# Performance work log

Measured on AMD Instinct MI355X. Metric: run time of the kernel, lower is better.

## Reference

```python
import jax, jax.numpy as jnp
import numpy as np

CD_WT = 5.0
CLASSIFY_WT = 1.0
B, N, M, NUM_CLASSES = 32, 2048, 2048, 6


def setup_inputs() -> dict:
    key = jax.random.key(0)
    k1, k2, k3, k4 = jax.random.split(key, 4)
    inst_shape = jax.random.normal(k1, (B, N, 3), dtype=jnp.float32)
    model = jax.random.normal(k2, (B, M, 3), dtype=jnp.float32)
    pred = jax.random.normal(k3, (B, NUM_CLASSES), dtype=jnp.float32)
    gt = jax.random.randint(k4, (B,), 0, NUM_CLASSES, dtype=jnp.int64)
    return {"inst_shape": inst_shape, "model": model, "pred": pred, "gt": gt}


def _chamfer(a, b):
    # a: [B,N,3], b: [B,M,3]; squared pairwise distances [B,N,M]
    # ||a-b||^2 = ||a||^2 + ||b||^2 - 2 a.b  (avoids [B,N,M,3] intermediate)
    a2 = jnp.sum(a * a, axis=-1)  # [B,N]
    b2 = jnp.sum(b * b, axis=-1)  # [B,M]
    ab = jnp.einsum('bnd,bmd->bnm', a, b)  # [B,N,M]
    d = a2[:, :, None] + b2[:, None, :] - 2.0 * ab  # [B,N,M]
    dist1 = jnp.min(d, axis=2)  # [B,N] nearest in b for each a
    dist2 = jnp.min(d, axis=1)  # [B,M] nearest in a for each b
    loss = jnp.mean(dist1) + jnp.mean(dist2)
    return loss, dist1, dist2


def _cross_entropy(logits, labels):
    # nn.CrossEntropyLoss with default mean reduction
    logp = jax.nn.log_softmax(logits, axis=-1)  # [B,C]
    nll = -jnp.take_along_axis(logp, labels[:, None], axis=-1)[:, 0]
    return jnp.mean(nll)


def reference(inst_shape, model, pred, gt):
    cd_loss, _, _ = _chamfer(inst_shape, model)
    classify_loss = _cross_entropy(pred, gt)
    total_loss = CD_WT * cd_loss + CLASSIFY_WT * classify_loss
    return (total_loss, cd_loss, classify_loss)
```

## Files before the change

### kernel.cpp

```cpp
#include <hip/hip_runtime.h>

typedef __attribute__((ext_vector_type(8)))  short short8;
typedef __attribute__((ext_vector_type(16))) float f32x16;
typedef __attribute__((ext_vector_type(16))) unsigned u32x16;

#define NPTS 2048
#define BATCH 32
#define NUM_CLASSES 6
#define THREADS 256
#define BF16_ONE ((short)0x3F80)
#define FMAX_BITS 0x7F7FFFFFu

__device__ __forceinline__ unsigned short f2bf(float x) {
    union { float f; unsigned u; } v; v.f = x;
    unsigned r = v.u + 0x7FFF + ((v.u >> 16) & 1);
    return (unsigned short)(r >> 16);
}
__device__ __forceinline__ float bf2f(unsigned short h) {
    union { unsigned u; float f; } v; v.u = ((unsigned)h) << 16; return v.f;
}
__device__ __forceinline__ unsigned f2u(float x) {
    union { float f; unsigned u; } v; v.f = x; return v.u;
}
__device__ __forceinline__ float u2f(unsigned x) {
    union { unsigned u; float f; } v; v.u = x; return v.f;
}
__device__ __forceinline__ unsigned umin2(unsigned a, unsigned b) {
    return a < b ? a : b;
}
template<int CTRL>
__device__ __forceinline__ unsigned dpp_ror_umin(unsigned v) {
    unsigned r = (unsigned)__builtin_amdgcn_update_dpp((int)v, (int)v, CTRL, 0xF, 0xF, false);
    return umin2(v, r);
}
__device__ __forceinline__ unsigned swz16_umin(unsigned v) {
    unsigned r = (unsigned)__builtin_amdgcn_ds_swizzle((int)v, 0x401F);
    return umin2(v, r);
}

__global__ __launch_bounds__(THREADS, 2) void chamfer_mfma32(
    const float* __restrict__ inst, const float* __restrict__ model,
    float* __restrict__ partial)
{
    __shared__ char  cands[NPTS * 32];
    __shared__ float wsum[4];

    const int blk   = blockIdx.x;
    const int dir   = blk >> 8;
    const int batch = (blk >> 3) & 31;
    const int qc    = blk & 7;
    const int tid   = threadIdx.x;
    const int lane  = tid & 63, wid = tid >> 6;
    const int lh    = lane >> 5, lr = lane & 31;

    const float* __restrict__ Q = dir ? model : inst;
    const float* __restrict__ C = dir ? inst  : model;

    const float* cb = C + (size_t)batch * NPTS * 3;
    for (int c = tid; c < NPTS; c += THREADS) {
        float bx = cb[c*3+0], by = cb[c*3+1], bz = cb[c*3+2];
        float m2x = -2.f*bx, m2y = -2.f*by, m2z = -2.f*bz;
        unsigned short hx = f2bf(m2x), hy = f2bf(m2y), hz = f2bf(m2z);
        unsigned short lx = f2bf(m2x - bf2f(hx));
        unsigned short ly = f2bf(m2y - bf2f(hy));
        unsigned short lz = f2bf(m2z - bf2f(hz));
        float b2 = fmaf(bx,bx, fmaf(by,by, bz*bz));
        unsigned short b2h = f2bf(b2);
        unsigned short b2l = f2bf(b2 - bf2f(b2h));
        short8 kg0 = { (short)hx,(short)hy,(short)hz,(short)hx,(short)hy,(short)hz,(short)lx,(short)ly };
        short8 kg1 = { (short)lz,(short)b2h,(short)b2l, BF16_ONE, BF16_ONE, 0,0,0 };
        char* tbase = cands + (c >> 5) * 1024 + (c & 31) * 16;
        *(short8*)(tbase)       = kg0;
        *(short8*)(tbase + 512) = kg1;
    }

    short8 af0, af1;
    const float* qb = Q + ((size_t)batch * NPTS + (size_t)qc * 256) * 3;
    #pragma unroll
    for (int qt = 0; qt < 2; ++qt) {
        const int qi = (wid * 2 + qt) * 32 + lr;
        float x = qb[qi*3+0], y = qb[qi*3+1], z = qb[qi*3+2];
        unsigned short hx = f2bf(x), hy = f2bf(y), hz = f2bf(z);
        unsigned short lx = f2bf(x - bf2f(hx));
        unsigned short ly = f2bf(y - bf2f(hy));
        unsigned short lz = f2bf(z - bf2f(hz));
        float a2 = fmaf(x,x, fmaf(y,y, z*z));
        unsigned short a2h = f2bf(a2);
        unsigned short a2l = f2bf(a2 - bf2f(a2h));
        short8 f;
        if (lh == 0)
            f = (short8){ (short)hx,(short)hy,(short)hz,(short)lx,(short)ly,(short)lz,(short)hx,(short)hy };
        else
            f = (short8){ (short)hz, BF16_ONE, BF16_ONE, (short)a2h,(short)a2l, 0,0,0 };
        if (qt == 0) af0 = f; else af1 = f;
    }
    __syncthreads();

    u32x16 mnU, mnU2;
    f32x16 zero16;
    #pragma unroll
    for (int r = 0; r < 16; ++r) { mnU[r] = FMAX_BITS; mnU2[r] = FMAX_BITS; zero16[r] = 0.f; }

    const char* cp = cands + lh * 512 + lr * 16;
    short8 c0 = *(const short8*)(cp);
    short8 c1 = *(const short8*)(cp + 1024);
    short8 n0 = *(const short8*)(cp + 2048);
    short8 n1 = *(const short8*)(cp + 3072);
    cp += 4096;
    f32x16 p00 = __builtin_amdgcn_mfma_f32_32x32x16_bf16(af0, c0, zero16, 0,0,0);
    f32x16 p01 = __builtin_amdgcn_mfma_f32_32x32x16_bf16(af0, c1, zero16, 0,0,0);
    f32x16 p10 = __builtin_amdgcn_mfma_f32_32x32x16_bf16(af1, c0, zero16, 0,0,0);
    f32x16 p11 = __builtin_amdgcn_mfma_f32_32x32x16_bf16(af1, c1, zero16, 0,0,0);

    #pragma unroll 2
    for (int s = 1; s < 31; ++s) {
        c0 = n0; c1 = n1;
        n0 = *(const short8*)(cp);
        n1 = *(const short8*)(cp + 1024);
        cp += 2048;
        f32x16 q00 = __builtin_amdgcn_mfma_f32_32x32x16_bf16(af0, c0, zero16, 0,0,0);
        f32x16 q01 = __builtin_amdgcn_mfma_f32_32x32x16_bf16(af0, c1, zero16, 0,0,0);
        f32x16 q10 = __builtin_amdgcn_mfma_f32_32x32x16_bf16(af1, c0, zero16, 0,0,0);
        f32x16 q11 = __builtin_amdgcn_mfma_f32_32x32x16_bf16(af1, c1, zero16, 0,0,0);
        #pragma unroll
        for (int r = 0; r < 16; ++r)
            mnU[r]  = umin2(umin2(f2u(p00[r]), f2u(p01[r])), mnU[r]);
        #pragma unroll
        for (int r = 0; r < 16; ++r)
            mnU2[r] = umin2(umin2(f2u(p10[r]), f2u(p11[r])), mnU2[r]);
        p00 = q00; p01 = q01; p10 = q10; p11 = q11;
    }
    {
        f32x16 q00 = __builtin_amdgcn_mfma_f32_32x32x16_bf16(af0, n0, zero16, 0,0,0);
        f32x16 q01 = __builtin_amdgcn_mfma_f32_32x32x16_bf16(af0, n1, zero16, 0,0,0);
        f32x16 q10 = __builtin_amdgcn_mfma_f32_32x32x16_bf16(af1, n0, zero16, 0,0,0);
        f32x16 q11 = __builtin_amdgcn_mfma_f32_32x32x16_bf16(af1, n1, zero16, 0,0,0);
        #pragma unroll
        for (int r = 0; r < 16; ++r) {
            mnU[r]  = umin2(umin2(f2u(p00[r]), f2u(p01[r])), mnU[r]);
            mnU2[r] = umin2(umin2(f2u(p10[r]), f2u(p11[r])), mnU2[r]);
        }
        #pragma unroll
        for (int r = 0; r < 16; ++r) {
            mnU[r]  = umin2(umin2(f2u(q00[r]), f2u(q01[r])), mnU[r]);
            mnU2[r] = umin2(umin2(f2u(q10[r]), f2u(q11[r])), mnU2[r]);
        }
    }

    float s = 0.f;
    #pragma unroll
    for (int r = 0; r < 16; ++r) {
        unsigned v = mnU[r];
        v = dpp_ror_umin<0x121>(v);
        v = dpp_ror_umin<0x122>(v);
        v = dpp_ror_umin<0x124>(v);
        v = dpp_ror_umin<0x128>(v);
        v = swz16_umin(v);
        s += u2f(v);
        unsigned w = mnU2[r];
        w = dpp_ror_umin<0x121>(w);
        w = dpp_ror_umin<0x122>(w);
        w = dpp_ror_umin<0x124>(w);
        w = dpp_ror_umin<0x128>(w);
        w = swz16_umin(w);
        s += u2f(w);
    }
    s += __shfl_xor(s, 32, 64);
    if (lane == 0) wsum[wid] = s;
    __syncthreads();
    if (tid == 0) partial[blk] = (wsum[0] + wsum[1]) + (wsum[2] + wsum[3]);
}

__global__ __launch_bounds__(256) void finalize_kernel(
    const float* __restrict__ partial, const float* __restrict__ pred,
    const int* __restrict__ gt, float* __restrict__ out)
{
    __shared__ float s_ce[BATCH];
    __shared__ float wsum[4];
    const int tid = threadIdx.x;

    float v = partial[tid] + partial[tid + 256];
    #pragma unroll
    for (int o = 32; o > 0; o >>= 1) v += __shfl_down(v, o, 64);
    const int lane = tid & 63, wid = tid >> 6;
    if (lane == 0) wsum[wid] = v;

    if (tid < BATCH) {
        const float* row = pred + tid * NUM_CLASSES;
        float mx = row[0];
        #pragma unroll
        for (int c = 1; c < NUM_CLASSES; ++c) mx = fmaxf(mx, row[c]);
        float se = 0.f;
        #pragma unroll
        for (int c = 0; c < NUM_CLASSES; ++c) se += __expf(row[c] - mx);
        const int lbl = gt[tid];
        s_ce[tid] = -(row[lbl] - mx - __logf(se));
    }
    __syncthreads();

    if (tid == 0) {
        float cd_sum = (wsum[0] + wsum[1]) + (wsum[2] + wsum[3]);
        float cd = cd_sum / (float)(BATCH * NPTS);
        float ce = 0.f;
        for (int i = 0; i < BATCH; ++i) ce += s_ce[i];
        ce /= (float)BATCH;
        out[0] = 5.f * cd + ce;
        out[1] = cd;
        out[2] = ce;
    }
}

extern "C" void kernel_launch(void* const* d_in, const int* in_sizes, int n_in,
                              void* d_out, int out_size, void* d_ws, size_t ws_size,
                              hipStream_t stream) {
    const float* inst  = (const float*)d_in[0];
    const float* model = (const float*)d_in[1];
    const float* pred  = (const float*)d_in[2];
    const int*   gt    = (const int*)d_in[3];
    float* out     = (float*)d_out;
    float* partial = (float*)d_ws;

    chamfer_mfma32<<<512, THREADS, 0, stream>>>(inst, model, partial);
    finalize_kernel<<<1, 256, 0, stream>>>(partial, pred, gt, out);
}
```

Before: 17.86 us.

## Compute the distance matrix once and derive row and column minima with atomics

Instead of launching separate block sets for each chamfer direction, each block now computes one tile of the inst-by-model distance matrix. It folds row minima and column minima from the same MFMA outputs and merges them into global buffers with atomicMin. This halves the MFMA and LDS candidate work. In exchange it adds a memset of the min buffers, per-step cross-lane shuffles and global atomics, plus an extra reduction kernel launch before the finalize step.

```diff
diff --git a/kernel.cpp b/kernel.cpp
--- a/kernel.cpp
+++ b/kernel.cpp
@@ -11,6 +11,9 @@
 #define BF16_ONE ((short)0x3F80)
 #define FMAX_BITS 0x7F7FFFFFu
 
+#define COL_OFF  65536
+#define PART_OFF 131072
+
 __device__ __forceinline__ unsigned short f2bf(float x) {
     union { float f; unsigned u; } v; v.f = x;
     unsigned r = v.u + 0x7FFF + ((v.u >> 16) & 1);
@@ -38,26 +41,27 @@
     return umin2(v, r);
 }
 
-__global__ __launch_bounds__(THREADS, 2) void chamfer_mfma32(
+__global__ __launch_bounds__(THREADS, 2) void chamfer_sym(
     const float* __restrict__ inst, const float* __restrict__ model,
-    float* __restrict__ partial)
+    unsigned* __restrict__ ws)
 {
-    __shared__ char  cands[NPTS * 32];
-    __shared__ float wsum[4];
+    __shared__ char cands[1024 * 32];
 
     const int blk   = blockIdx.x;
-    const int dir   = blk >> 8;
-    const int batch = (blk >> 3) & 31;
-    const int qc    = blk & 7;
+    const int mc    = blk & 1;
+    const int qc    = (blk >> 1) & 7;
+    const int batch = blk >> 4;
     const int tid   = threadIdx.x;
     const int lane  = tid & 63, wid = tid >> 6;
     const int lh    = lane >> 5, lr = lane & 31;
 
-    const float* __restrict__ Q = dir ? model : inst;
-    const float* __restrict__ C = dir ? inst  : model;
-
-    const float* cb = C + (size_t)batch * NPTS * 3;
-    for (int c = tid; c < NPTS; c += THREADS) {
+    unsigned* rowmin = ws + batch * NPTS;
+    unsigned* colmin = ws + COL_OFF + batch * NPTS + mc * 1024;
+
+    const float* cb = model + ((size_t)batch * NPTS + (size_t)mc * 1024) * 3;
+    #pragma unroll
+    for (int k = 0; k < 4; ++k) {
+        const int c = tid + k * THREADS;
         float bx = cb[c*3+0], by = cb[c*3+1], bz = cb[c*3+2];
         float m2x = -2.f*bx, m2y = -2.f*by, m2z = -2.f*bz;
         unsigned short hx = f2bf(m2x), hy = f2bf(m2y), hz = f2bf(m2z);
@@ -75,7 +79,7 @@
     }
 
     short8 af0, af1;
-    const float* qb = Q + ((size_t)batch * NPTS + (size_t)qc * 256) * 3;
+    const float* qb = inst + ((size_t)batch * NPTS + (size_t)qc * 256) * 3;
     #pragma unroll
     for (int qt = 0; qt < 2; ++qt) {
         const int qi = (wid * 2 + qt) * 32 + lr;
@@ -101,6 +105,25 @@
     #pragma unroll
     for (int r = 0; r < 16; ++r) { mnU[r] = FMAX_BITS; mnU2[r] = FMAX_BITS; zero16[r] = 0.f; }
 
+#define FOLD(P00,P01,P10,P11, TB) do {                                         \
+    _Pragma("unroll") for (int r = 0; r < 16; ++r)                             \
+        mnU[r]  = umin2(umin2(f2u(P00[r]), f2u(P01[r])), mnU[r]);              \
+    _Pragma("unroll") for (int r = 0; r < 16; ++r)                             \
+        mnU2[r] = umin2(umin2(f2u(P10[r]), f2u(P11[r])), mnU2[r]);             \
+    unsigned ca = umin2(f2u(P00[0]), f2u(P10[0]));                             \
+    unsigned cc = umin2(f2u(P01[0]), f2u(P11[0]));                             \
+    _Pragma("unroll") for (int r = 1; r < 16; ++r) {                           \
+        ca = umin2(ca, umin2(f2u(P00[r]), f2u(P10[r])));                       \
+        cc = umin2(cc, umin2(f2u(P01[r]), f2u(P11[r])));                       \
+    }                                                                          \
+    ca = umin2(ca, (unsigned)__shfl_xor((int)ca, 32, 64));                     \
+    cc = umin2(cc, (unsigned)__shfl_xor((int)cc, 32, 64));                     \
+    if (lh == 0) {                                                             \
+        atomicMin(&colmin[(TB) + lr], ca);                                     \
+        atomicMin(&colmin[(TB) + 32 + lr], cc);                                \
+    }                                                                          \
+} while (0)
+
     const char* cp = cands + lh * 512 + lr * 16;
     short8 c0 = *(const short8*)(cp);
     short8 c1 = *(const short8*)(cp + 1024);
@@ -113,7 +136,7 @@
     f32x16 p11 = __builtin_amdgcn_mfma_f32_32x32x16_bf16(af1, c1, zero16, 0,0,0);
 
     #pragma unroll 2
-    for (int s = 1; s < 31; ++s) {
+    for (int s = 1; s < 15; ++s) {
         c0 = n0; c1 = n1;
         n0 = *(const short8*)(cp);
         n1 = *(const short8*)(cp + 1024);
@@ -122,12 +145,7 @@
         f32x16 q01 = __builtin_amdgcn_mfma_f32_32x32x16_bf16(af0, c1, zero16, 0,0,0);
         f32x16 q10 = __builtin_amdgcn_mfma_f32_32x32x16_bf16(af1, c0, zero16, 0,0,0);
         f32x16 q11 = __builtin_amdgcn_mfma_f32_32x32x16_bf16(af1, c1, zero16, 0,0,0);
-        #pragma unroll
-        for (int r = 0; r < 16; ++r)
-            mnU[r]  = umin2(umin2(f2u(p00[r]), f2u(p01[r])), mnU[r]);
-        #pragma unroll
-        for (int r = 0; r < 16; ++r)
-            mnU2[r] = umin2(umin2(f2u(p10[r]), f2u(p11[r])), mnU2[r]);
+        FOLD(p00, p01, p10, p11, (s - 1) * 64);
         p00 = q00; p01 = q01; p10 = q10; p11 = q11;
     }
     {
@@ -135,55 +153,59 @@
         f32x16 q01 = __builtin_amdgcn_mfma_f32_32x32x16_bf16(af0, n1, zero16, 0,0,0);
         f32x16 q10 = __builtin_amdgcn_mfma_f32_32x32x16_bf16(af1, n0, zero16, 0,0,0);
         f32x16 q11 = __builtin_amdgcn_mfma_f32_32x32x16_bf16(af1, n1, zero16, 0,0,0);
-        #pragma unroll
-        for (int r = 0; r < 16; ++r) {
-            mnU[r]  = umin2(umin2(f2u(p00[r]), f2u(p01[r])), mnU[r]);
-            mnU2[r] = umin2(umin2(f2u(p10[r]), f2u(p11[r])), mnU2[r]);
-        }
-        #pragma unroll
-        for (int r = 0; r < 16; ++r) {
-            mnU[r]  = umin2(umin2(f2u(q00[r]), f2u(q01[r])), mnU[r]);
-            mnU2[r] = umin2(umin2(f2u(q10[r]), f2u(q11[r])), mnU2[r]);
-        }
-    }
-
-    float s = 0.f;
+        FOLD(p00, p01, p10, p11, 14 * 64);
+        FOLD(q00, q01, q10, q11, 15 * 64);
+    }
+#undef FOLD
+
     #pragma unroll
     for (int r = 0; r < 16; ++r) {
+        const int crow = (r & 3) + 8 * (r >> 2) + 4 * lh;
         unsigned v = mnU[r];
         v = dpp_ror_umin<0x121>(v);
         v = dpp_ror_umin<0x122>(v);
         v = dpp_ror_umin<0x124>(v);
         v = dpp_ror_umin<0x128>(v);
         v = swz16_umin(v);
-        s += u2f(v);
+        if (lr == 0) atomicMin(&rowmin[qc*256 + (wid*2+0)*32 + crow], v);
         unsigned w = mnU2[r];
         w = dpp_ror_umin<0x121>(w);
         w = dpp_ror_umin<0x122>(w);
         w = dpp_ror_umin<0x124>(w);
         w = dpp_ror_umin<0x128>(w);
         w = swz16_umin(w);
-        s += u2f(w);
-    }
-    s += __shfl_xor(s, 32, 64);
+        if (lr == 0) atomicMin(&rowmin[qc*256 + (wid*2+1)*32 + crow], w);
+    }
+}
+
+__global__ __launch_bounds__(256) void reduce_kernel(
+    const unsigned* __restrict__ ws, float* __restrict__ partial)
+{
+    const int b   = blockIdx.x;
+    const int tid = threadIdx.x;
+    const unsigned* base = ws + (size_t)b * NPTS;
+    float s = 0.f;
+    #pragma unroll
+    for (int k = 0; k < 8; ++k) s += u2f(base[k * 256 + tid]);
+    #pragma unroll
+    for (int o = 32; o > 0; o >>= 1) s += __shfl_down(s, o, 64);
+    __shared__ float wsum[4];
+    const int lane = tid & 63, wid = tid >> 6;
     if (lane == 0) wsum[wid] = s;
     __syncthreads();
-    if (tid == 0) partial[blk] = (wsum[0] + wsum[1]) + (wsum[2] + wsum[3]);
-}
-
-__global__ __launch_bounds__(256) void finalize_kernel(
+    if (tid == 0) partial[b] = (wsum[0] + wsum[1]) + (wsum[2] + wsum[3]);
+}
+
+__global__ __launch_bounds__(64) void finalize_kernel(
     const float* __restrict__ partial, const float* __restrict__ pred,
     const int* __restrict__ gt, float* __restrict__ out)
 {
+    const int tid = threadIdx.x;
     __shared__ float s_ce[BATCH];
-    __shared__ float wsum[4];
-    const int tid = threadIdx.x;
-
-    float v = partial[tid] + partial[tid + 256];
+
+    float v = partial[tid];
     #pragma unroll
     for (int o = 32; o > 0; o >>= 1) v += __shfl_down(v, o, 64);
-    const int lane = tid & 63, wid = tid >> 6;
-    if (lane == 0) wsum[wid] = v;
 
     if (tid < BATCH) {
         const float* row = pred + tid * NUM_CLASSES;
@@ -199,8 +221,7 @@
     __syncthreads();
 
     if (tid == 0) {
-        float cd_sum = (wsum[0] + wsum[1]) + (wsum[2] + wsum[3]);
-        float cd = cd_sum / (float)(BATCH * NPTS);
+        float cd = v / (float)(BATCH * NPTS);
         float ce = 0.f;
         for (int i = 0; i < BATCH; ++i) ce += s_ce[i];
         ce /= (float)BATCH;
@@ -217,9 +238,11 @@
     const float* model = (const float*)d_in[1];
     const float* pred  = (const float*)d_in[2];
     const int*   gt    = (const int*)d_in[3];
-    float* out     = (float*)d_out;
-    float* partial = (float*)d_ws;
-
-    chamfer_mfma32<<<512, THREADS, 0, stream>>>(inst, model, partial);
-    finalize_kernel<<<1, 256, 0, stream>>>(partial, pred, gt, out);
-}
+    float* out = (float*)d_out;
+    unsigned* ws = (unsigned*)d_ws;
+
+    hipMemsetAsync(d_ws, 0x7F, (size_t)PART_OFF * sizeof(unsigned), stream);
+    chamfer_sym<<<512, THREADS, 0, stream>>>(inst, model, ws);
+    reduce_kernel<<<64, 256, 0, stream>>>(ws, (float*)(ws + PART_OFF));
+    finalize_kernel<<<1, 64, 0, stream>>>((float*)(ws + PART_OFF), pred, gt, out);
+}
```

New measurement: 30.13 us. 1.69x slower.

## Precompute bf16 candidate image in prep kernel and stream it into LDS via global_load_lds

Applied to the files above, without the earlier changes.

Adds a prep kernel that converts each candidate point set into the split-bf16 MFMA operand layout once per batch and direction, writing it to workspace. The main kernel then copies this prebuilt image directly into LDS using global_load_lds instead of having each of its 8 blocks per batch recompute the conversion and scatter it to LDS. This removes redundant conversion work and LDS store overhead. In exchange it adds an extra kernel launch and a 4 MB workspace write and read.

```diff
diff --git a/kernel.cpp b/kernel.cpp
--- a/kernel.cpp
+++ b/kernel.cpp
@@ -11,6 +11,8 @@
 #define BF16_ONE ((short)0x3F80)
 #define FMAX_BITS 0x7F7FFFFFu
 
+#define BIMG_BYTES (64u * 2048u * 32u)
+
 __device__ __forceinline__ unsigned short f2bf(float x) {
     union { float f; unsigned u; } v; v.f = x;
     unsigned r = v.u + 0x7FFF + ((v.u >> 16) & 1);
@@ -37,10 +39,42 @@
     unsigned r = (unsigned)__builtin_amdgcn_ds_swizzle((int)v, 0x401F);
     return umin2(v, r);
 }
+__device__ __forceinline__ void gload_lds16(const char* g, char* l) {
+    __builtin_amdgcn_global_load_lds(
+        (__attribute__((address_space(1))) void*)(g),
+        (__attribute__((address_space(3))) void*)(l), 16, 0, 0);
+}
+
+__global__ __launch_bounds__(256) void prep_kernel(
+    const float* __restrict__ inst, const float* __restrict__ model,
+    char* __restrict__ bimg)
+{
+    const int idx      = blockIdx.x * 256 + threadIdx.x;
+    const int dirbatch = idx >> 11;
+    const int c        = idx & 2047;
+    const int dir      = dirbatch >> 5;
+    const int batch    = dirbatch & 31;
+
+    const float* src = (dir ? inst : model) + ((size_t)batch * NPTS + c) * 3;
+    float bx = src[0], by = src[1], bz = src[2];
+    float m2x = -2.f*bx, m2y = -2.f*by, m2z = -2.f*bz;
+    unsigned short hx = f2bf(m2x), hy = f2bf(m2y), hz = f2bf(m2z);
+    unsigned short lx = f2bf(m2x - bf2f(hx));
+    unsigned short ly = f2bf(m2y - bf2f(hy));
+    unsigned short lz = f2bf(m2z - bf2f(hz));
+    float b2 = fmaf(bx,bx, fmaf(by,by, bz*bz));
+    unsigned short b2h = f2bf(b2);
+    unsigned short b2l = f2bf(b2 - bf2f(b2h));
+    short8 kg0 = { (short)hx,(short)hy,(short)hz,(short)hx,(short)hy,(short)hz,(short)lx,(short)ly };
+    short8 kg1 = { (short)lz,(short)b2h,(short)b2l, BF16_ONE, BF16_ONE, 0,0,0 };
+    char* dst = bimg + (size_t)dirbatch * 65536 + (c >> 5) * 1024 + (c & 31) * 16;
+    *(short8*)(dst)       = kg0;
+    *(short8*)(dst + 512) = kg1;
+}
 
 __global__ __launch_bounds__(THREADS, 2) void chamfer_mfma32(
     const float* __restrict__ inst, const float* __restrict__ model,
-    float* __restrict__ partial)
+    const char* __restrict__ bimg, float* __restrict__ partial)
 {
     __shared__ char  cands[NPTS * 32];
     __shared__ float wsum[4];
@@ -52,28 +86,17 @@
     const int tid   = threadIdx.x;
     const int lane  = tid & 63, wid = tid >> 6;
     const int lh    = lane >> 5, lr = lane & 31;
+    const int dirbatch = dir * BATCH + batch;
+
+    {
+        const char* g = bimg + (size_t)dirbatch * 65536 + wid * 16384 + lane * 16;
+        char* l = cands + wid * 16384;
+        #pragma unroll
+        for (int j = 0; j < 16; ++j)
+            gload_lds16(g + j * 1024, l + j * 1024);
+    }
 
     const float* __restrict__ Q = dir ? model : inst;
-    const float* __restrict__ C = dir ? inst  : model;
-
-    const float* cb = C + (size_t)batch * NPTS * 3;
-    for (int c = tid; c < NPTS; c += THREADS) {
-        float bx = cb[c*3+0], by = cb[c*3+1], bz = cb[c*3+2];
-        float m2x = -2.f*bx, m2y = -2.f*by, m2z = -2.f*bz;
-        unsigned short hx = f2bf(m2x), hy = f2bf(m2y), hz = f2bf(m2z);
-        unsigned short lx = f2bf(m2x - bf2f(hx));
-        unsigned short ly = f2bf(m2y - bf2f(hy));
-        unsigned short lz = f2bf(m2z - bf2f(hz));
-        float b2 = fmaf(bx,bx, fmaf(by,by, bz*bz));
-        unsigned short b2h = f2bf(b2);
-        unsigned short b2l = f2bf(b2 - bf2f(b2h));
-        short8 kg0 = { (short)hx,(short)hy,(short)hz,(short)hx,(short)hy,(short)hz,(short)lx,(short)ly };
-        short8 kg1 = { (short)lz,(short)b2h,(short)b2l, BF16_ONE, BF16_ONE, 0,0,0 };
-        char* tbase = cands + (c >> 5) * 1024 + (c & 31) * 16;
-        *(short8*)(tbase)       = kg0;
-        *(short8*)(tbase + 512) = kg1;
-    }
-
     short8 af0, af1;
     const float* qb = Q + ((size_t)batch * NPTS + (size_t)qc * 256) * 3;
     #pragma unroll
@@ -217,9 +240,11 @@
     const float* model = (const float*)d_in[1];
     const float* pred  = (const float*)d_in[2];
     const int*   gt    = (const int*)d_in[3];
-    float* out     = (float*)d_out;
-    float* partial = (float*)d_ws;
-
-    chamfer_mfma32<<<512, THREADS, 0, stream>>>(inst, model, partial);
+    float* out  = (float*)d_out;
+    char*  bimg = (char*)d_ws;
+    float* partial = (float*)((char*)d_ws + BIMG_BYTES);
+
+    prep_kernel<<<512, 256, 0, stream>>>(inst, model, bimg);
+    chamfer_mfma32<<<512, THREADS, 0, stream>>>(inst, model, bimg, partial);
     finalize_kernel<<<1, 256, 0, stream>>>(partial, pred, gt, out);
 }
```

Measured after the change: 27.11 us. 51.8% more time.
